# Performance work log

Hardware: AMD Instinct MI355X
Metric: run time of the kernel (lower is better)

The kernel has to match this reference:

```python
import jax, jax.numpy as jnp
import numpy as np

BS = 512          # number of nodes (batch)
EMBED = 256       # embed_dim
NHEAD = 8
HDIM = EMBED // NHEAD
E = BS * BS       # fully-connected intra-batch graph


def _xavier(key, shape):
    lim = float(np.sqrt(6.0 / (shape[0] + shape[1])))
    return jax.random.uniform(key, shape, jnp.float32, -lim, lim)


def setup_inputs() -> dict:
    key = jax.random.key(0)
    ks = jax.random.split(key, 6)
    feats = jax.random.normal(ks[0], (BS, EMBED), jnp.float32)
    # edges sorted by destination c, exactly BS edges per destination
    dst = jnp.repeat(jnp.arange(BS), BS)   # c
    src = jnp.tile(jnp.arange(BS), BS)     # r
    edge_index = jnp.stack([src, dst], axis=1).astype(jnp.int32)  # [E, 2], cols (r, c)
    edge_attr = jnp.zeros((E, 1), jnp.float32)  # unused by forward
    return {
        "feats": feats,
        "edge_index": edge_index,
        "edge_attr": edge_attr,
        "Wq": _xavier(ks[1], (EMBED, EMBED)), "bq": jnp.zeros((EMBED,), jnp.float32),
        "Wk": _xavier(ks[2], (EMBED, EMBED)), "bk": jnp.zeros((EMBED,), jnp.float32),
        "Wv": _xavier(ks[3], (EMBED, EMBED)), "bv": jnp.zeros((EMBED,), jnp.float32),
        "Wo": _xavier(ks[4], (EMBED, EMBED)), "bo": jnp.zeros((EMBED,), jnp.float32),
    }


def reference(feats, edge_index, edge_attr, Wq, bq, Wk, bk, Wv, bv, Wo, bo):
    bs = feats.shape[0]
    scale = 1.0 / np.sqrt(HDIM)
    # QKV projections (torch Linear: x @ W.T + b), split heads -> [h, n, d]
    q = (feats @ Wq.T + bq).reshape(bs, NHEAD, HDIM).transpose(1, 0, 2)
    k = (feats @ Wk.T + bk).reshape(bs, NHEAD, HDIM).transpose(1, 0, 2)
    v = (feats @ Wv.T + bv).reshape(bs, NHEAD, HDIM).transpose(1, 0, 2)
    r, c = edge_index[:, 0], edge_index[:, 1]
    qe = q[:, c, :]   # [h, E, d] query of destination node
    ke = k[:, r, :]   # [h, E, d] key of source node
    ve = v[:, r, :]   # [h, E, d] value of source node
    sim = jnp.einsum('hed,hed->eh', qe, ke) * scale   # [E, h]
    # deterministic segment softmax over edges grouped by destination c
    m = jax.ops.segment_max(sim, c, num_segments=bs)  # [n, h]
    p = jnp.exp(sim - m[c])
    s = jax.ops.segment_sum(p, c, num_segments=bs)    # [n, h]
    attn = p / s[c]                                    # [E, h]
    # weight values and scatter-add per destination (aggr='add')
    out_e = attn.T[..., None] * ve                     # [h, E, d]
    out_e = out_e.transpose(1, 0, 2).reshape(-1, NHEAD * HDIM)  # [E, h*d]
    agg = jax.ops.segment_sum(out_e, c, num_segments=bs)        # [n, embed]
    return agg @ Wo.T + bo
```

## Files before the change

kernel.cpp:

```cpp
#include <hip/hip_runtime.h>

#define BS 512
#define EMBED 256
#define NHEAD 8
#define HDIM 32

typedef __attribute__((ext_vector_type(8))) short short8;
typedef __attribute__((ext_vector_type(4))) float f32x4;

__device__ inline f32x4 mfma16(short8 a, short8 b, f32x4 c) {
    return __builtin_amdgcn_mfma_f32_16x16x32_bf16(a, b, c, 0, 0, 0);
}

__device__ inline unsigned short f2bf(float x) {
    unsigned int u = __float_as_uint(x);
    u += 0x7FFFu + ((u >> 16) & 1u);
    return (unsigned short)(u >> 16);
}
__device__ inline float bf2f(unsigned short h) {
    return __uint_as_float(((unsigned int)h) << 16);
}
__device__ inline void split8(const float* p, short8& hi, short8& lo) {
    float4 a = *(const float4*)p;
    float4 b = *(const float4*)(p + 4);
    float x[8] = {a.x, a.y, a.z, a.w, b.x, b.y, b.z, b.w};
#pragma unroll
    for (int j = 0; j < 8; ++j) {
        unsigned short h = f2bf(x[j]);
        hi[j] = (short)h;
        lo[j] = (short)f2bf(x[j] - bf2f(h));
    }
}

__global__ __launch_bounds__(256) void qkv_fused(
    const float* __restrict__ feats,
    const float* __restrict__ Wq, const float* __restrict__ Wk,
    const float* __restrict__ Wv,
    const float* __restrict__ bq, const float* __restrict__ bk,
    const float* __restrict__ bv,
    unsigned short* __restrict__ Qhi, unsigned short* __restrict__ Qlo,
    unsigned short* __restrict__ Khi, unsigned short* __restrict__ Klo,
    unsigned short* __restrict__ Vthi, unsigned short* __restrict__ Vtlo,
    float* __restrict__ OUT)
{
    const int gidx = blockIdx.x * 256 + threadIdx.x;
    if (gidx < 32768) {
        float4 z = {0.f, 0.f, 0.f, 0.f};
        ((float4*)OUT)[gidx] = z;
    }

    const int wave = blockIdx.x * 4 + (threadIdx.x >> 6);
    const int l = threadIdx.x & 63;
    const int r = l & 15, g = l >> 4;
    const int nt = wave % 48, mt = wave / 48;
    const int m0 = mt * 16, n0 = nt * 16;
    const int seg = n0 >> 8;
    const int nn = n0 & 255;
    const float* W = (seg == 0) ? Wq : (seg == 1) ? Wk : Wv;
    const float* bias = (seg == 0) ? bq : (seg == 1) ? bk : bv;

    const float* arow = feats + (m0 + r) * EMBED;
    const float* brow = W + (nn + r) * EMBED;

    f32x4 acc = {0.f, 0.f, 0.f, 0.f};
#pragma unroll
    for (int kb = 0; kb < 8; ++kb) {
        const int k0 = kb * 32 + g * 8;
        short8 ah, al, bh, bl;
        split8(arow + k0, ah, al);
        split8(brow + k0, bh, bl);
        acc = mfma16(ah, bh, acc);
        acc = mfma16(ah, bl, acc);
        acc = mfma16(al, bh, acc);
    }
    const float bb = bias[nn + r];

    if (seg < 2) {
        unsigned short* Dhi = seg ? Khi : Qhi;
        unsigned short* Dlo = seg ? Klo : Qlo;
#pragma unroll
        for (int r4 = 0; r4 < 4; ++r4) {
            const int i = m0 + g * 4 + r4;
            const int c = nn + r;
            float v = acc[r4] + bb;
            unsigned short hh = f2bf(v);
            Dhi[i * EMBED + c] = hh;
            Dlo[i * EMBED + c] = f2bf(v - bf2f(hh));
        }
    } else {
        const int c = nn + r;
        const int i0 = m0 + g * 4;
        ushort4 ph, pl;
        float v0 = acc[0] + bb, v1 = acc[1] + bb;
        float v2 = acc[2] + bb, v3 = acc[3] + bb;
        ph.x = f2bf(v0); ph.y = f2bf(v1); ph.z = f2bf(v2); ph.w = f2bf(v3);
        pl.x = f2bf(v0 - bf2f(ph.x)); pl.y = f2bf(v1 - bf2f(ph.y));
        pl.z = f2bf(v2 - bf2f(ph.z)); pl.w = f2bf(v3 - bf2f(ph.w));
        *(ushort4*)(Vthi + c * BS + i0) = ph;
        *(ushort4*)(Vtlo + c * BS + i0) = pl;
    }
}

__global__ __launch_bounds__(512) void attn_out(
    const unsigned short* __restrict__ Qhi, const unsigned short* __restrict__ Qlo,
    const unsigned short* __restrict__ Khi, const unsigned short* __restrict__ Klo,
    const unsigned short* __restrict__ Vthi, const unsigned short* __restrict__ Vtlo,
    const float* __restrict__ Wo, const float* __restrict__ bo,
    float* __restrict__ OUT)
{
    const int qt = blockIdx.x >> 3;
    const int h = blockIdx.x & 7;
    const int q0 = qt * 16;
    const int tid = threadIdx.x;
    const int w = tid >> 6, l = tid & 63;
    const int r = l & 15, g = l >> 4;

    __shared__ unsigned short Psm[16 * 512];
    __shared__ float Opart[8][2][256];
    __shared__ float Rpart[8][16];
    __shared__ float Agg[16][36];
    char* Pb = (char*)Psm;

    const short8 qhi = *(const short8*)(Qhi + (q0 + r) * EMBED + h * HDIM + g * 8);
    const short8 qlo = *(const short8*)(Qlo + (q0 + r) * EMBED + h * HDIM + g * 8);

    const float cs = 0.17677669529663687f;
    float rs[4] = {0.f, 0.f, 0.f, 0.f};

#pragma unroll
    for (int kt = 0; kt < 4; ++kt) {
        const int krow = w * 64 + kt * 16 + r;
        short8 kh = *(const short8*)(Khi + krow * EMBED + h * HDIM + g * 8);
        short8 kl = *(const short8*)(Klo + krow * EMBED + h * HDIM + g * 8);
        f32x4 acc = {0.f, 0.f, 0.f, 0.f};
        acc = mfma16(qhi, kh, acc);
        acc = mfma16(qhi, kl, acc);
        acc = mfma16(qlo, kh, acc);
#pragma unroll
        for (int r4 = 0; r4 < 4; ++r4) {
            float p = __expf(acc[r4] * cs);
            rs[r4] += p;
            const int q = g * 4 + r4;
            const int bofs = q * 1024 + ((krow * 2) ^ ((q & 7) << 4));
            *(unsigned short*)(Pb + bofs) = f2bf(p);
        }
    }
#pragma unroll
    for (int off = 1; off < 16; off <<= 1) {
#pragma unroll
        for (int r4 = 0; r4 < 4; ++r4) rs[r4] += __shfl_xor(rs[r4], off);
    }
    if (r == 0) {
#pragma unroll
        for (int r4 = 0; r4 < 4; ++r4) Rpart[w][g * 4 + r4] = rs[r4];
    }

    f32x4 o0 = {0.f, 0.f, 0.f, 0.f}, o1 = {0.f, 0.f, 0.f, 0.f};
    const unsigned short* V0h = Vthi + (h * HDIM + r) * BS;
    const unsigned short* V0l = Vtlo + (h * HDIM + r) * BS;
    const unsigned short* V1h = V0h + 16 * BS;
    const unsigned short* V1l = V0l + 16 * BS;
#pragma unroll
    for (int kc = 0; kc < 2; ++kc) {
        const int kb = w * 64 + kc * 32 + g * 8;
        const int bofs = r * 1024 + ((kb * 2) ^ ((r & 7) << 4));
        short8 pa = *(const short8*)(Pb + bofs);
        o0 = mfma16(pa, *(const short8*)(V0h + kb), o0);
        o0 = mfma16(pa, *(const short8*)(V0l + kb), o0);
        o1 = mfma16(pa, *(const short8*)(V1h + kb), o1);
        o1 = mfma16(pa, *(const short8*)(V1l + kb), o1);
    }
    ((f32x4*)&Opart[w][0][0])[l] = o0;
    ((f32x4*)&Opart[w][1][0])[l] = o1;
    __syncthreads();

    if (w < 2) {
        f32x4 o = ((f32x4*)&Opart[0][w][0])[l];
#pragma unroll
        for (int p = 1; p < 8; ++p) {
            f32x4 t = ((f32x4*)&Opart[p][w][0])[l];
            o[0] += t[0]; o[1] += t[1]; o[2] += t[2]; o[3] += t[3];
        }
#pragma unroll
        for (int r4 = 0; r4 < 4; ++r4) {
            const int q = g * 4 + r4;
            float rt = Rpart[0][q];
#pragma unroll
            for (int p = 1; p < 8; ++p) rt += Rpart[p][q];
            Agg[q][w * 16 + r] = o[r4] / rt;
        }
    }
    __syncthreads();

    short8 ah, al;
    split8(&Agg[r][g * 8], ah, al);
#pragma unroll
    for (int nsub = 0; nsub < 2; ++nsub) {
        const int j0 = w * 32 + nsub * 16;
        short8 bh, bl;
        split8(Wo + (j0 + r) * EMBED + h * HDIM + g * 8, bh, bl);
        f32x4 a = {0.f, 0.f, 0.f, 0.f};
        a = mfma16(ah, bh, a);
        a = mfma16(ah, bl, a);
        a = mfma16(al, bh, a);
#pragma unroll
        for (int r4 = 0; r4 < 4; ++r4) {
            const int row = q0 + g * 4 + r4;
            const int col = j0 + r;
            float v = a[r4];
            if (h == 0) v += bo[col];
            atomicAdd(&OUT[row * EMBED + col], v);
        }
    }
}

extern "C" void kernel_launch(void* const* d_in, const int* in_sizes, int n_in,
                              void* d_out, int out_size, void* d_ws, size_t ws_size,
                              hipStream_t stream) {
    const float* feats = (const float*)d_in[0];
    const float* Wq = (const float*)d_in[3];
    const float* bq = (const float*)d_in[4];
    const float* Wk = (const float*)d_in[5];
    const float* bk = (const float*)d_in[6];
    const float* Wv = (const float*)d_in[7];
    const float* bv = (const float*)d_in[8];
    const float* Wo = (const float*)d_in[9];
    const float* bo = (const float*)d_in[10];
    float* out = (float*)d_out;

    unsigned short* ws = (unsigned short*)d_ws;
    const size_t NE = (size_t)BS * EMBED;
    unsigned short* Qhi  = ws;
    unsigned short* Qlo  = Qhi + NE;
    unsigned short* Khi  = Qlo + NE;
    unsigned short* Klo  = Khi + NE;
    unsigned short* Vthi = Klo + NE;
    unsigned short* Vtlo = Vthi + NE;

    qkv_fused<<<384, 256, 0, stream>>>(feats, Wq, Wk, Wv, bq, bk, bv,
                                       Qhi, Qlo, Khi, Klo, Vthi, Vtlo, out);
    attn_out<<<256, 512, 0, stream>>>(Qhi, Qlo, Khi, Klo, Vthi, Vtlo,
                                      Wo, bo, out);
}
```

Before: 26.15 us.

## Use 32x32 QKV tiles, head-major Q/K, drop V low part, pre-split Wo

The QKV projection now computes a 32x32 tile per wave with four accumulators, reusing each split A/B fragment across two MFMAs, and launches 96 blocks instead of 384. Q and K are stored head-major so the attention kernel reads contiguous per-head rows. The low-order bf16 part of V is dropped, halving the P·V MFMAs and V traffic at some cost in precision. Wo is split into hi/lo bf16 in the first kernel so the output projection loads bf16 directly instead of converting in every block. Fewer blocks in the first kernel lowers parallelism, and dropping the V correction may affect the accuracy tolerance.

```diff
diff --git a/kernel.cpp b/kernel.cpp
--- a/kernel.cpp
+++ b/kernel.cpp
@@ -35,78 +35,112 @@
 __global__ __launch_bounds__(256) void qkv_fused(
     const float* __restrict__ feats,
     const float* __restrict__ Wq, const float* __restrict__ Wk,
-    const float* __restrict__ Wv,
+    const float* __restrict__ Wv, const float* __restrict__ Wo,
     const float* __restrict__ bq, const float* __restrict__ bk,
     const float* __restrict__ bv,
     unsigned short* __restrict__ Qhi, unsigned short* __restrict__ Qlo,
     unsigned short* __restrict__ Khi, unsigned short* __restrict__ Klo,
-    unsigned short* __restrict__ Vthi, unsigned short* __restrict__ Vtlo,
+    unsigned short* __restrict__ Vthi,
+    unsigned short* __restrict__ Wohi, unsigned short* __restrict__ Wolo,
     float* __restrict__ OUT)
 {
     const int gidx = blockIdx.x * 256 + threadIdx.x;
-    if (gidx < 32768) {
+
+    for (int j = gidx; j < 32768; j += 24576) {
         float4 z = {0.f, 0.f, 0.f, 0.f};
-        ((float4*)OUT)[gidx] = z;
+        ((float4*)OUT)[j] = z;
+    }
+    for (int j = gidx; j < 16384; j += 24576) {
+        float4 v = ((const float4*)Wo)[j];
+        const int jrow = j >> 6;
+        const int c4 = (j & 63) * 4;
+        const int head = c4 >> 5, dim = c4 & 31;
+        const int dst = head * (EMBED * HDIM) + jrow * HDIM + dim;
+        ushort4 ph, pl;
+        ph.x = f2bf(v.x); pl.x = f2bf(v.x - bf2f(ph.x));
+        ph.y = f2bf(v.y); pl.y = f2bf(v.y - bf2f(ph.y));
+        ph.z = f2bf(v.z); pl.z = f2bf(v.z - bf2f(ph.z));
+        ph.w = f2bf(v.w); pl.w = f2bf(v.w - bf2f(ph.w));
+        *(ushort4*)(Wohi + dst) = ph;
+        *(ushort4*)(Wolo + dst) = pl;
     }
 
     const int wave = blockIdx.x * 4 + (threadIdx.x >> 6);
     const int l = threadIdx.x & 63;
     const int r = l & 15, g = l >> 4;
-    const int nt = wave % 48, mt = wave / 48;
-    const int m0 = mt * 16, n0 = nt * 16;
+    const int nt = wave % 24, mt = wave / 24;
+    const int m0 = mt * 32, n0 = nt * 32;
     const int seg = n0 >> 8;
     const int nn = n0 & 255;
     const float* W = (seg == 0) ? Wq : (seg == 1) ? Wk : Wv;
     const float* bias = (seg == 0) ? bq : (seg == 1) ? bk : bv;
 
-    const float* arow = feats + (m0 + r) * EMBED;
-    const float* brow = W + (nn + r) * EMBED;
-
-    f32x4 acc = {0.f, 0.f, 0.f, 0.f};
+    const float* a0 = feats + (m0 + r) * EMBED;
+    const float* a1 = a0 + 16 * EMBED;
+    const float* b0 = W + (nn + r) * EMBED;
+    const float* b1 = b0 + 16 * EMBED;
+
+    f32x4 acc00 = {0,0,0,0}, acc01 = {0,0,0,0}, acc10 = {0,0,0,0}, acc11 = {0,0,0,0};
 #pragma unroll
     for (int kb = 0; kb < 8; ++kb) {
         const int k0 = kb * 32 + g * 8;
-        short8 ah, al, bh, bl;
-        split8(arow + k0, ah, al);
-        split8(brow + k0, bh, bl);
-        acc = mfma16(ah, bh, acc);
-        acc = mfma16(ah, bl, acc);
-        acc = mfma16(al, bh, acc);
-    }
-    const float bb = bias[nn + r];
-
-    if (seg < 2) {
-        unsigned short* Dhi = seg ? Khi : Qhi;
-        unsigned short* Dlo = seg ? Klo : Qlo;
-#pragma unroll
-        for (int r4 = 0; r4 < 4; ++r4) {
-            const int i = m0 + g * 4 + r4;
-            const int c = nn + r;
-            float v = acc[r4] + bb;
-            unsigned short hh = f2bf(v);
-            Dhi[i * EMBED + c] = hh;
-            Dlo[i * EMBED + c] = f2bf(v - bf2f(hh));
-        }
-    } else {
-        const int c = nn + r;
-        const int i0 = m0 + g * 4;
-        ushort4 ph, pl;
-        float v0 = acc[0] + bb, v1 = acc[1] + bb;
-        float v2 = acc[2] + bb, v3 = acc[3] + bb;
-        ph.x = f2bf(v0); ph.y = f2bf(v1); ph.z = f2bf(v2); ph.w = f2bf(v3);
-        pl.x = f2bf(v0 - bf2f(ph.x)); pl.y = f2bf(v1 - bf2f(ph.y));
-        pl.z = f2bf(v2 - bf2f(ph.z)); pl.w = f2bf(v3 - bf2f(ph.w));
-        *(ushort4*)(Vthi + c * BS + i0) = ph;
-        *(ushort4*)(Vtlo + c * BS + i0) = pl;
+        short8 A0h, A0l, A1h, A1l, B0h, B0l, B1h, B1l;
+        split8(a0 + k0, A0h, A0l);
+        split8(a1 + k0, A1h, A1l);
+        split8(b0 + k0, B0h, B0l);
+        split8(b1 + k0, B1h, B1l);
+        acc00 = mfma16(A0h, B0h, acc00);
+        acc01 = mfma16(A0h, B1h, acc01);
+        acc10 = mfma16(A1h, B0h, acc10);
+        acc11 = mfma16(A1h, B1h, acc11);
+        acc00 = mfma16(A0h, B0l, acc00);
+        acc01 = mfma16(A0h, B1l, acc01);
+        acc10 = mfma16(A1h, B0l, acc10);
+        acc11 = mfma16(A1h, B1l, acc11);
+        acc00 = mfma16(A0l, B0h, acc00);
+        acc01 = mfma16(A0l, B1h, acc01);
+        acc10 = mfma16(A1l, B0h, acc10);
+        acc11 = mfma16(A1l, B1h, acc11);
+    }
+
+#pragma unroll
+    for (int ti = 0; ti < 2; ++ti) {
+#pragma unroll
+        for (int tj = 0; tj < 2; ++tj) {
+            f32x4 a = (ti == 0) ? (tj == 0 ? acc00 : acc01)
+                                : (tj == 0 ? acc10 : acc11);
+            const int cn = nn + tj * 16 + r;
+            const float bb = bias[cn];
+            if (seg < 2) {
+                unsigned short* Dhi = seg ? Khi : Qhi;
+                unsigned short* Dlo = seg ? Klo : Qlo;
+                const int head = cn >> 5, dim = cn & 31;
+#pragma unroll
+                for (int r4 = 0; r4 < 4; ++r4) {
+                    const int i = m0 + ti * 16 + g * 4 + r4;
+                    float v = a[r4] + bb;
+                    unsigned short hh = f2bf(v);
+                    const int addr = head * (BS * HDIM) + i * HDIM + dim;
+                    Dhi[addr] = hh;
+                    Dlo[addr] = f2bf(v - bf2f(hh));
+                }
+            } else {
+                const int i0 = m0 + ti * 16 + g * 4;
+                ushort4 ph;
+                ph.x = f2bf(a[0] + bb); ph.y = f2bf(a[1] + bb);
+                ph.z = f2bf(a[2] + bb); ph.w = f2bf(a[3] + bb);
+                *(ushort4*)(Vthi + cn * BS + i0) = ph;
+            }
+        }
     }
 }
 
 __global__ __launch_bounds__(512) void attn_out(
     const unsigned short* __restrict__ Qhi, const unsigned short* __restrict__ Qlo,
     const unsigned short* __restrict__ Khi, const unsigned short* __restrict__ Klo,
-    const unsigned short* __restrict__ Vthi, const unsigned short* __restrict__ Vtlo,
-    const float* __restrict__ Wo, const float* __restrict__ bo,
-    float* __restrict__ OUT)
+    const unsigned short* __restrict__ Vthi,
+    const unsigned short* __restrict__ Wohi, const unsigned short* __restrict__ Wolo,
+    const float* __restrict__ bo, float* __restrict__ OUT)
 {
     const int qt = blockIdx.x >> 3;
     const int h = blockIdx.x & 7;
@@ -121,8 +155,10 @@
     __shared__ float Agg[16][36];
     char* Pb = (char*)Psm;
 
-    const short8 qhi = *(const short8*)(Qhi + (q0 + r) * EMBED + h * HDIM + g * 8);
-    const short8 qlo = *(const short8*)(Qlo + (q0 + r) * EMBED + h * HDIM + g * 8);
+    const unsigned short* Kh = Khi + h * (BS * HDIM);
+    const unsigned short* Kl = Klo + h * (BS * HDIM);
+    const short8 qhi = *(const short8*)(Qhi + h * (BS * HDIM) + (q0 + r) * HDIM + g * 8);
+    const short8 qlo = *(const short8*)(Qlo + h * (BS * HDIM) + (q0 + r) * HDIM + g * 8);
 
     const float cs = 0.17677669529663687f;
     float rs[4] = {0.f, 0.f, 0.f, 0.f};
@@ -130,8 +166,8 @@
 #pragma unroll
     for (int kt = 0; kt < 4; ++kt) {
         const int krow = w * 64 + kt * 16 + r;
-        short8 kh = *(const short8*)(Khi + krow * EMBED + h * HDIM + g * 8);
-        short8 kl = *(const short8*)(Klo + krow * EMBED + h * HDIM + g * 8);
+        short8 kh = *(const short8*)(Kh + krow * HDIM + g * 8);
+        short8 kl = *(const short8*)(Kl + krow * HDIM + g * 8);
         f32x4 acc = {0.f, 0.f, 0.f, 0.f};
         acc = mfma16(qhi, kh, acc);
         acc = mfma16(qhi, kl, acc);
@@ -157,18 +193,14 @@
 
     f32x4 o0 = {0.f, 0.f, 0.f, 0.f}, o1 = {0.f, 0.f, 0.f, 0.f};
     const unsigned short* V0h = Vthi + (h * HDIM + r) * BS;
-    const unsigned short* V0l = Vtlo + (h * HDIM + r) * BS;
     const unsigned short* V1h = V0h + 16 * BS;
-    const unsigned short* V1l = V0l + 16 * BS;
 #pragma unroll
     for (int kc = 0; kc < 2; ++kc) {
         const int kb = w * 64 + kc * 32 + g * 8;
         const int bofs = r * 1024 + ((kb * 2) ^ ((r & 7) << 4));
         short8 pa = *(const short8*)(Pb + bofs);
         o0 = mfma16(pa, *(const short8*)(V0h + kb), o0);
-        o0 = mfma16(pa, *(const short8*)(V0l + kb), o0);
         o1 = mfma16(pa, *(const short8*)(V1h + kb), o1);
-        o1 = mfma16(pa, *(const short8*)(V1l + kb), o1);
     }
     ((f32x4*)&Opart[w][0][0])[l] = o0;
     ((f32x4*)&Opart[w][1][0])[l] = o1;
@@ -194,11 +226,13 @@
 
     short8 ah, al;
     split8(&Agg[r][g * 8], ah, al);
+    const unsigned short* Woh = Wohi + h * (EMBED * HDIM);
+    const unsigned short* Wol = Wolo + h * (EMBED * HDIM);
 #pragma unroll
     for (int nsub = 0; nsub < 2; ++nsub) {
         const int j0 = w * 32 + nsub * 16;
-        short8 bh, bl;
-        split8(Wo + (j0 + r) * EMBED + h * HDIM + g * 8, bh, bl);
+        short8 bh = *(const short8*)(Woh + (j0 + r) * HDIM + g * 8);
+        short8 bl = *(const short8*)(Wol + (j0 + r) * HDIM + g * 8);
         f32x4 a = {0.f, 0.f, 0.f, 0.f};
         a = mfma16(ah, bh, a);
         a = mfma16(ah, bl, a);
@@ -230,15 +264,18 @@
 
     unsigned short* ws = (unsigned short*)d_ws;
     const size_t NE = (size_t)BS * EMBED;
+    const size_t WO = (size_t)EMBED * EMBED;
     unsigned short* Qhi  = ws;
     unsigned short* Qlo  = Qhi + NE;
     unsigned short* Khi  = Qlo + NE;
     unsigned short* Klo  = Khi + NE;
     unsigned short* Vthi = Klo + NE;
-    unsigned short* Vtlo = Vthi + NE;
-
-    qkv_fused<<<384, 256, 0, stream>>>(feats, Wq, Wk, Wv, bq, bk, bv,
-                                       Qhi, Qlo, Khi, Klo, Vthi, Vtlo, out);
-    attn_out<<<256, 512, 0, stream>>>(Qhi, Qlo, Khi, Klo, Vthi, Vtlo,
-                                      Wo, bo, out);
-}
+    unsigned short* Wohi = Vthi + NE;
+    unsigned short* Wolo = Wohi + WO;
+
+    qkv_fused<<<96, 256, 0, stream>>>(feats, Wq, Wk, Wv, Wo, bq, bk, bv,
+                                      Qhi, Qlo, Khi, Klo, Vthi,
+                                      Wohi, Wolo, out);
+    attn_out<<<256, 512, 0, stream>>>(Qhi, Qlo, Khi, Klo, Vthi,
+                                      Wohi, Wolo, bo, out);
+}
```

Result: faster. 24.86 us (-5.0%).
